# Kernel optimization log

Hardware: AMD Instinct MI355X
Metric: run time of the kernel (lower is better)

## Reference

```python
import jax, jax.numpy as jnp
import numpy as np

N_CAMS = 6
Y, X, Z = 8, 256, 256      # voxel grid (height, x, z)
H, W = 224, 400            # image size used by project_world2img scale
XV, ZV = 56, 100           # img_feats spatial dims [BS,C,XV,ZV]
EPS = 1e-6


def setup_inputs():
    key = jax.random.key(0)
    k1, k2, k3 = jax.random.split(key, 3)
    BS, C = N_CAMS, 32
    img_feats = jax.random.normal(k1, (BS, C, XV, ZV), jnp.float32)
    variances = jax.random.uniform(k2, (BS, 1, H, W), jnp.float32)
    render_depth = jax.random.uniform(k3, (BS, 1, H, W), jnp.float32) * 50.0
    # voxel sample coords, ordering matches crop_base: (x_patch, z_patch, height)
    hs = jnp.linspace(-1.0, 3.0, Y)
    xs = jnp.linspace(-24.0, 24.0, X)
    zs = jnp.linspace(-24.0, 24.0, Z)
    hh, px, pz = jnp.meshgrid(hs, xs, zs, indexing='ij')
    sample_coords = jnp.stack([px, pz, hh], -1).reshape(1, Y * X * Z, 3)
    # six surround cameras at origin, yaw-rotated, looking horizontally (cam2world)
    Ps = np.zeros((N_CAMS, 4, 4), np.float32)
    for i in range(N_CAMS):
        a = i * (2.0 * np.pi / N_CAMS)
        c, s = np.cos(a), np.sin(a)
        # columns are camera x/y/z axes in world coords (y down, z forward)
        Ps[i, :3, :3] = np.array([[s, 0.0, c], [-c, 0.0, s], [0.0, -1.0, 0.0]], np.float32)
        Ps[i, 3, 3] = 1.0
    Ks = np.tile(np.array([[250.0, 0.0, W / 2.0], [0.0, 250.0, H / 2.0], [0.0, 0.0, 1.0]],
                          np.float32), (N_CAMS, 1, 1))
    return {"img_feats": img_feats, "variances": variances, "render_depth": render_depth,
            "sample_coords": sample_coords, "Ps": jnp.asarray(Ps), "Ks": jnp.asarray(Ks)}


def _grid_sample_2d(feat, gx, gy):
    # feat [BS,C,Hf,Wf]; gx,gy [BS,N] normalized to [-1,1].
    # torch.grid_sample bilinear, padding_mode='zeros', align_corners=False
    BS, C, Hf, Wf = feat.shape
    x = (gx + 1.0) * (Wf * 0.5) - 0.5
    y = (gy + 1.0) * (Hf * 0.5) - 0.5
    x0 = jnp.floor(x)
    y0 = jnp.floor(y)
    wx, wy = x - x0, y - y0
    flat = feat.reshape(BS, C, Hf * Wf)
    out = jnp.zeros((BS, C, gx.shape[1]), feat.dtype)
    for dx, dy, wgt in ((0, 0, (1 - wx) * (1 - wy)), (1, 0, wx * (1 - wy)),
                        (0, 1, (1 - wx) * wy), (1, 1, wx * wy)):
        xi = x0 + dx
        yi = y0 + dy
        valid = (xi >= 0) & (xi < Wf) & (yi >= 0) & (yi < Hf)
        idx = (jnp.clip(yi, 0, Hf - 1) * Wf + jnp.clip(xi, 0, Wf - 1)).astype(jnp.int32)
        v = jnp.take_along_axis(flat, idx[:, None, :], axis=2)  # [BS,C,N]
        out = out + v * (wgt * valid)[:, None, :]
    return out


def _masked_mean(x, m, axis):
    # reduce_masked_mean: sum(x*m)/ (sum(m)+eps) along axis
    return jnp.sum(x * m, axis=axis) / (jnp.sum(m, axis=axis) + EPS)


def reference(img_feats, variances, render_depth, sample_coords, Ps, Ks):
    BS, C = img_feats.shape[:2]
    B = BS // N_CAMS
    N = sample_coords.shape[1]
    # --- project_world2img: world -> cam -> pixel ---
    pts_h = jnp.concatenate([sample_coords, jnp.ones((1, N, 1), sample_coords.dtype)], -1)
    w2c = jnp.linalg.inv(Ps)                                    # [BS,4,4]
    cam = jnp.einsum('bij,anj->bni', w2c[:, :3, :], pts_h)      # [BS,N,3]
    uvw = jnp.einsum('bij,bnj->bni', Ks, cam)                   # [BS,N,3]
    zc = uvw[..., 2]
    zsafe = jnp.where(jnp.abs(zc) < 1e-6, 1e-6, zc)
    u = uvw[..., 0] / zsafe
    v = uvw[..., 1] / zsafe
    pix = jnp.nan_to_num(jnp.stack([v, u], -1), nan=-1.0)       # (row, col), scale (H, W)
    mask = (zc > 1e-3) & (u >= 0) & (u < W) & (v >= 0) & (v < H)
    # samp_ind = pix / [H, W] * 2 - 1; coord0 indexes width of permuted feat
    gx = pix[..., 0] / H * 2.0 - 1.0
    gy = pix[..., 1] / W * 2.0 - 1.0
    mf = mask.reshape(B, N_CAMS, 1, Y, X, Z).astype(img_feats.dtype)
    # feature lift: grid_sample on img_feats.permute(0,1,3,2) -> [BS,C,ZV,XV]
    out = _grid_sample_2d(jnp.swapaxes(img_feats, 2, 3), gx, gy)
    out = out.reshape(B, N_CAMS, C, Y, X, Z)
    out_feats = _masked_mean(out, mf, 1).reshape(B, C * Y, X, Z)
    # variance info branch
    var = _grid_sample_2d(jnp.swapaxes(variances, 2, 3), gx, gy)
    var_info = _masked_mean(var.reshape(B, N_CAMS, 1, Y, X, Z), mf, 1).reshape(B, Y, X, Z)
    # depth info branch
    nd = _grid_sample_2d(jnp.swapaxes(render_depth, 2, 3), gx, gy)
    nerf_depth = _masked_mean(nd.reshape(B, N_CAMS, 1, Y, X, Z), mf, 1)  # [B,1,Y,X,Z]
    depth = _masked_mean(zc.reshape(B, N_CAMS, 1, Y, X, Z), mf, 1)       # [B,1,Y,X,Z]
    return (out_feats, var_info, depth, nerf_depth)
```

## Files before the change

### kernel.cpp

```cpp
#include <hip/hip_runtime.h>
#include <math.h>

#define NCAMS 6
#define CCH   32
#define YY    8
#define XX    256
#define ZZ    256
#define NVOX  (YY*XX*ZZ)
#define IMG_H 224
#define IMG_W 400
#define FXV   56
#define FZV   100

#define NF (NCAMS*FXV*FZV)
#define NV (NCAMS*IMG_H*IMG_W)
#define FEATS_T_ELEMS (NF*CCH)
#define VD_T_ELEMS    (NV*2)
#define WS_NEED_BYTES ((size_t)(FEATS_T_ELEMS + VD_T_ELEMS) * 4)

__global__ __launch_bounds__(256) void prep_all(
    const float* __restrict__ src_f, const float* __restrict__ var,
    const float* __restrict__ dep, float* __restrict__ dst_f,
    float* __restrict__ dst_vd)
{
    int t = blockIdx.x * 256 + threadIdx.x;
    if (t < NF) {
        int b = t / (FXV * FZV);
        int r = t - b * (FXV * FZV);
        float4* d4 = (float4*)(dst_f + (size_t)t * CCH);
        #pragma unroll
        for (int j = 0; j < CCH / 4; j++) {
            float4 v;
            v.x = src_f[(size_t)(b * CCH + 4*j + 0) * (FXV*FZV) + r];
            v.y = src_f[(size_t)(b * CCH + 4*j + 1) * (FXV*FZV) + r];
            v.z = src_f[(size_t)(b * CCH + 4*j + 2) * (FXV*FZV) + r];
            v.w = src_f[(size_t)(b * CCH + 4*j + 3) * (FXV*FZV) + r];
            d4[j] = v;
        }
    } else {
        int u = t - NF;
        if (u < NV) ((float2*)dst_vd)[u] = make_float2(var[u], dep[u]);
    }
}

__global__ __launch_bounds__(128) void mvmap_fast(
    const float* __restrict__ feats_t,
    const float* __restrict__ vd_t,
    const float* __restrict__ coords,
    const float* __restrict__ Ps,
    const float* __restrict__ Ks,
    float* __restrict__ out)
{
    __shared__ float4 sW2C[NCAMS][3];
    __shared__ float4 sK[NCAMS][3];

    if (threadIdx.x < NCAMS) {
        int b = threadIdx.x;
        const float* P = Ps + b * 16;
        float r00=P[0], r01=P[1], r02=P[2],  tx=P[3];
        float r10=P[4], r11=P[5], r12=P[6],  ty=P[7];
        float r20=P[8], r21=P[9], r22=P[10], tz=P[11];
        float det = r00*(r11*r22 - r12*r21)
                  - r01*(r10*r22 - r12*r20)
                  + r02*(r10*r21 - r11*r20);
        float id = 1.0f / det;
        float i00 =  (r11*r22 - r12*r21) * id;
        float i01 = -(r01*r22 - r02*r21) * id;
        float i02 =  (r01*r12 - r02*r11) * id;
        float i10 = -(r10*r22 - r12*r20) * id;
        float i11 =  (r00*r22 - r02*r20) * id;
        float i12 = -(r00*r12 - r02*r10) * id;
        float i20 =  (r10*r21 - r11*r20) * id;
        float i21 = -(r00*r21 - r01*r20) * id;
        float i22 =  (r00*r11 - r01*r10) * id;
        sW2C[b][0] = make_float4(i00, i01, i02, -(i00*tx + i01*ty + i02*tz));
        sW2C[b][1] = make_float4(i10, i11, i12, -(i10*tx + i11*ty + i12*tz));
        sW2C[b][2] = make_float4(i20, i21, i22, -(i20*tx + i21*ty + i22*tz));
        sK[b][0] = make_float4(Ks[b*9+0], Ks[b*9+1], Ks[b*9+2], 0.f);
        sK[b][1] = make_float4(Ks[b*9+3], Ks[b*9+4], Ks[b*9+5], 0.f);
        sK[b][2] = make_float4(Ks[b*9+6], Ks[b*9+7], Ks[b*9+8], 0.f);
    }
    __syncthreads();

    int t = blockIdx.x * 128 + threadIdx.x;
    int n = t >> 1;
    int j = t & 1;

    float px = coords[3*n + 0];
    float pz = coords[3*n + 1];
    float ph = coords[3*n + 2];

    float4 facc[4];
    #pragma unroll
    for (int q = 0; q < 4; q++) facc[q] = make_float4(0.f,0.f,0.f,0.f);
    float wsum = 0.0f, vsum = 0.0f, ndsum = 0.0f, zsum = 0.0f;

    int   nvis = 0;
    float s_u[3] = {0.f, 0.f, 0.f};
    float s_v[3] = {0.f, 0.f, 0.f};
    int   s_b[3] = {0, 0, 0};

    #pragma unroll
    for (int b = 0; b < NCAMS; b++) {
        float4 r0 = sW2C[b][0], r1 = sW2C[b][1], r2 = sW2C[b][2];
        float cx = r0.x*px + r0.y*pz + r0.z*ph + r0.w;
        float cy = r1.x*px + r1.y*pz + r1.z*ph + r1.w;
        float cz = r2.x*px + r2.y*pz + r2.z*ph + r2.w;
        float4 k0 = sK[b][0], k1 = sK[b][1], k2 = sK[b][2];
        float u0 = k0.x*cx + k0.y*cy + k0.z*cz;
        float v0 = k1.x*cx + k1.y*cy + k1.z*cz;
        float zc = k2.x*cx + k2.y*cy + k2.z*cz;
        float zsafe = (fabsf(zc) < 1e-6f) ? 1e-6f : zc;
        float u = u0 / zsafe;
        float v = v0 / zsafe;
        bool mask = (zc > 1e-3f) && (u >= 0.0f) && (u < (float)IMG_W)
                                 && (v >= 0.0f) && (v < (float)IMG_H);
        wsum += mask ? 1.0f : 0.0f;
        zsum += mask ? zc : 0.0f;
        bool c0 = mask && (nvis == 0);
        bool c1 = mask && (nvis == 1);
        bool c2 = mask && (nvis == 2);
        s_u[0] = c0 ? u : s_u[0];  s_v[0] = c0 ? v : s_v[0];  s_b[0] = c0 ? b : s_b[0];
        s_u[1] = c1 ? u : s_u[1];  s_v[1] = c1 ? v : s_v[1];  s_b[1] = c1 ? b : s_b[1];
        s_u[2] = c2 ? u : s_u[2];  s_v[2] = c2 ? v : s_v[2];  s_b[2] = c2 ? b : s_b[2];
        nvis += mask ? 1 : 0;
    }

    #pragma unroll
    for (int it = 0; it < 3; it++) {
        if (nvis > it) {
            float u = s_u[it], v = s_v[it];
            int   b = s_b[it];

            {
                float xf = v * 0.25f - 0.5f;
                float yf = u * 0.25f - 0.5f;
                float x0f = floorf(xf), y0f = floorf(yf);
                float wx = xf - x0f, wy = yf - y0f;
                int x0 = (int)x0f, y0 = (int)y0f;
                float vx0 = (x0   >= 0 && x0   < FXV) ? 1.0f : 0.0f;
                float vx1 = (x0+1 >= 0 && x0+1 < FXV) ? 1.0f : 0.0f;
                float vy0 = (y0   >= 0 && y0   < FZV) ? 1.0f : 0.0f;
                float vy1 = (y0+1 >= 0 && y0+1 < FZV) ? 1.0f : 0.0f;
                float w00 = (1.0f-wx)*(1.0f-wy)*vx0*vy0;
                float w10 = wx*(1.0f-wy)*vx1*vy0;
                float w01 = (1.0f-wx)*wy*vx0*vy1;
                float w11 = wx*wy*vx1*vy1;
                int xi0 = min(max(x0,   0), FXV-1), xi1 = min(max(x0+1, 0), FXV-1);
                int yi0 = min(max(y0,   0), FZV-1), yi1 = min(max(y0+1, 0), FZV-1);
                const float* base = feats_t + (size_t)b * (FXV*FZV*CCH) + j * 16;
                const float4* p00 = (const float4*)(base + (size_t)(xi0*FZV + yi0)*CCH);
                const float4* p01 = (const float4*)(base + (size_t)(xi0*FZV + yi1)*CCH);
                const float4* p10 = (const float4*)(base + (size_t)(xi1*FZV + yi0)*CCH);
                const float4* p11 = (const float4*)(base + (size_t)(xi1*FZV + yi1)*CCH);
                #pragma unroll
                for (int q = 0; q < 4; q++) {
                    float4 a = p00[q], b2 = p01[q], c2 = p10[q], d2 = p11[q];
                    facc[q].x += w00*a.x + w01*b2.x + w10*c2.x + w11*d2.x;
                    facc[q].y += w00*a.y + w01*b2.y + w10*c2.y + w11*d2.y;
                    facc[q].z += w00*a.z + w01*b2.z + w10*c2.z + w11*d2.z;
                    facc[q].w += w00*a.w + w01*b2.w + w10*c2.w + w11*d2.w;
                }
            }

            {
                float xf = v - 0.5f;
                float yf = u - 0.5f;
                float x0f = floorf(xf), y0f = floorf(yf);
                float wx = xf - x0f, wy = yf - y0f;
                int x0 = (int)x0f, y0 = (int)y0f;
                float vx0 = (x0   >= 0 && x0   < IMG_H) ? 1.0f : 0.0f;
                float vx1 = (x0+1 >= 0 && x0+1 < IMG_H) ? 1.0f : 0.0f;
                float vy0 = (y0   >= 0 && y0   < IMG_W) ? 1.0f : 0.0f;
                float vy1 = (y0+1 >= 0 && y0+1 < IMG_W) ? 1.0f : 0.0f;
                float w00 = (1.0f-wx)*(1.0f-wy)*vx0*vy0;
                float w10 = wx*(1.0f-wy)*vx1*vy0;
                float w01 = (1.0f-wx)*wy*vx0*vy1;
                float w11 = wx*wy*vx1*vy1;
                int xi0 = min(max(x0,   0), IMG_H-1), xi1 = min(max(x0+1, 0), IMG_H-1);
                int yi0 = min(max(y0,   0), IMG_W-1), yi1 = min(max(y0+1, 0), IMG_W-1);
                const float2* pv = (const float2*)(vd_t) + (size_t)b * (IMG_H*IMG_W);
                float2 t00 = pv[xi0*IMG_W + yi0], t01 = pv[xi0*IMG_W + yi1];
                float2 t10 = pv[xi1*IMG_W + yi0], t11 = pv[xi1*IMG_W + yi1];
                vsum  += w00*t00.x + w01*t01.x + w10*t10.x + w11*t11.x;
                ndsum += w00*t00.y + w01*t01.y + w10*t10.y + w11*t11.y;
            }
        }
    }

    float invd = 1.0f / (wsum + 1e-6f);
    #pragma unroll
    for (int q = 0; q < 4; q++) {
        #pragma unroll
        for (int k = 0; k < 4; k++) {
            float fv = (&facc[q].x)[k] * invd;
            __builtin_nontemporal_store(fv, &out[(size_t)(16*j + 4*q + k) * NVOX + n]);
        }
    }
    if (j == 0) {
        __builtin_nontemporal_store(vsum  * invd, &out[(size_t)CCH*NVOX + n]);
        __builtin_nontemporal_store(zsum  * invd, &out[(size_t)CCH*NVOX + NVOX + n]);
        __builtin_nontemporal_store(ndsum * invd, &out[(size_t)CCH*NVOX + 2*(size_t)NVOX + n]);
    }
}

__global__ __launch_bounds__(256) void mvmap_main(
    const float* __restrict__ img_feats,
    const float* __restrict__ variances,
    const float* __restrict__ render_depth,
    const float* __restrict__ coords,
    const float* __restrict__ Ps,
    const float* __restrict__ Ks,
    float* __restrict__ out)
{
    __shared__ float sW2C[NCAMS][12];
    __shared__ float sK[NCAMS][9];

    if (threadIdx.x < NCAMS) {
        int b = threadIdx.x;
        const float* P = Ps + b * 16;
        float r00=P[0], r01=P[1], r02=P[2],  tx=P[3];
        float r10=P[4], r11=P[5], r12=P[6],  ty=P[7];
        float r20=P[8], r21=P[9], r22=P[10], tz=P[11];
        float det = r00*(r11*r22 - r12*r21)
                  - r01*(r10*r22 - r12*r20)
                  + r02*(r10*r21 - r11*r20);
        float id = 1.0f / det;
        float i00 =  (r11*r22 - r12*r21) * id;
        float i01 = -(r01*r22 - r02*r21) * id;
        float i02 =  (r01*r12 - r02*r11) * id;
        float i10 = -(r10*r22 - r12*r20) * id;
        float i11 =  (r00*r22 - r02*r20) * id;
        float i12 = -(r00*r12 - r02*r10) * id;
        float i20 =  (r10*r21 - r11*r20) * id;
        float i21 = -(r00*r21 - r01*r20) * id;
        float i22 =  (r00*r11 - r01*r10) * id;
        sW2C[b][0]=i00; sW2C[b][1]=i01; sW2C[b][2] =i02; sW2C[b][3] =-(i00*tx + i01*ty + i02*tz);
        sW2C[b][4]=i10; sW2C[b][5]=i11; sW2C[b][6] =i12; sW2C[b][7] =-(i10*tx + i11*ty + i12*tz);
        sW2C[b][8]=i20; sW2C[b][9]=i21; sW2C[b][10]=i22; sW2C[b][11]=-(i20*tx + i21*ty + i22*tz);
        #pragma unroll
        for (int jj = 0; jj < 9; jj++) sK[b][jj] = Ks[b*9 + jj];
    }
    __syncthreads();

    int n = blockIdx.x * blockDim.x + threadIdx.x;
    if (n >= NVOX) return;

    float px = coords[3*n + 0];
    float pz = coords[3*n + 1];
    float ph = coords[3*n + 2];

    float fsum[CCH];
    #pragma unroll
    for (int c = 0; c < CCH; c++) fsum[c] = 0.0f;
    float wsum = 0.0f, vsum = 0.0f, ndsum = 0.0f, zsum = 0.0f;

    for (int b = 0; b < NCAMS; b++) {
        float cx = sW2C[b][0]*px + sW2C[b][1]*pz + sW2C[b][2] *ph + sW2C[b][3];
        float cy = sW2C[b][4]*px + sW2C[b][5]*pz + sW2C[b][6] *ph + sW2C[b][7];
        float cz = sW2C[b][8]*px + sW2C[b][9]*pz + sW2C[b][10]*ph + sW2C[b][11];
        float u0 = sK[b][0]*cx + sK[b][1]*cy + sK[b][2]*cz;
        float v0 = sK[b][3]*cx + sK[b][4]*cy + sK[b][5]*cz;
        float zc = sK[b][6]*cx + sK[b][7]*cy + sK[b][8]*cz;
        float zsafe = (fabsf(zc) < 1e-6f) ? 1e-6f : zc;
        float u = u0 / zsafe;
        float v = v0 / zsafe;
        bool mask = (zc > 1e-3f) && (u >= 0.0f) && (u < (float)IMG_W)
                                 && (v >= 0.0f) && (v < (float)IMG_H);
        if (!mask) continue;

        wsum += 1.0f;
        zsum += zc;
        {
            float xf = v * 0.25f - 0.5f;
            float yf = u * 0.25f - 0.5f;
            float x0f = floorf(xf), y0f = floorf(yf);
            float wx = xf - x0f, wy = yf - y0f;
            int x0 = (int)x0f, y0 = (int)y0f;
            float vx0 = (x0   >= 0 && x0   < FXV) ? 1.0f : 0.0f;
            float vx1 = (x0+1 >= 0 && x0+1 < FXV) ? 1.0f : 0.0f;
            float vy0 = (y0   >= 0 && y0   < FZV) ? 1.0f : 0.0f;
            float vy1 = (y0+1 >= 0 && y0+1 < FZV) ? 1.0f : 0.0f;
            float w00 = (1.0f-wx)*(1.0f-wy)*vx0*vy0;
            float w10 = wx*(1.0f-wy)*vx1*vy0;
            float w01 = (1.0f-wx)*wy*vx0*vy1;
            float w11 = wx*wy*vx1*vy1;
            int xi0 = min(max(x0,   0), FXV-1), xi1 = min(max(x0+1, 0), FXV-1);
            int yi0 = min(max(y0,   0), FZV-1), yi1 = min(max(y0+1, 0), FZV-1);
            int o00 = xi0*FZV + yi0, o01 = xi0*FZV + yi1;
            int o10 = xi1*FZV + yi0, o11 = xi1*FZV + yi1;
            const float* p = img_feats + (size_t)b * (CCH*FXV*FZV);
            #pragma unroll
            for (int c = 0; c < CCH; c++) {
                const float* pc = p + c * (FXV*FZV);
                fsum[c] += w00*pc[o00] + w01*pc[o01] + w10*pc[o10] + w11*pc[o11];
            }
        }
        {
            float xf = v - 0.5f;
            float yf = u - 0.5f;
            float x0f = floorf(xf), y0f = floorf(yf);
            float wx = xf - x0f, wy = yf - y0f;
            int x0 = (int)x0f, y0 = (int)y0f;
            float vx0 = (x0   >= 0 && x0   < IMG_H) ? 1.0f : 0.0f;
            float vx1 = (x0+1 >= 0 && x0+1 < IMG_H) ? 1.0f : 0.0f;
            float vy0 = (y0   >= 0 && y0   < IMG_W) ? 1.0f : 0.0f;
            float vy1 = (y0+1 >= 0 && y0+1 < IMG_W) ? 1.0f : 0.0f;
            float w00 = (1.0f-wx)*(1.0f-wy)*vx0*vy0;
            float w10 = wx*(1.0f-wy)*vx1*vy0;
            float w01 = (1.0f-wx)*wy*vx0*vy1;
            float w11 = wx*wy*vx1*vy1;
            int xi0 = min(max(x0,   0), IMG_H-1), xi1 = min(max(x0+1, 0), IMG_H-1);
            int yi0 = min(max(y0,   0), IMG_W-1), yi1 = min(max(y0+1, 0), IMG_W-1);
            int o00 = xi0*IMG_W + yi0, o01 = xi0*IMG_W + yi1;
            int o10 = xi1*IMG_W + yi0, o11 = xi1*IMG_W + yi1;
            const float* pv = variances    + (size_t)b * (IMG_H*IMG_W);
            const float* pd = render_depth + (size_t)b * (IMG_H*IMG_W);
            vsum  += w00*pv[o00] + w01*pv[o01] + w10*pv[o10] + w11*pv[o11];
            ndsum += w00*pd[o00] + w01*pd[o01] + w10*pd[o10] + w11*pd[o11];
        }
    }

    float invd = 1.0f / (wsum + 1e-6f);
    #pragma unroll
    for (int c = 0; c < CCH; c++) out[(size_t)c * NVOX + n] = fsum[c] * invd;
    out[(size_t)CCH*NVOX + n]              = vsum  * invd;
    out[(size_t)CCH*NVOX + NVOX + n]       = zsum  * invd;
    out[(size_t)CCH*NVOX + 2*(size_t)NVOX + n] = ndsum * invd;
}

extern "C" void kernel_launch(void* const* d_in, const int* in_sizes, int n_in,
                              void* d_out, int out_size, void* d_ws, size_t ws_size,
                              hipStream_t stream) {
    const float* img_feats    = (const float*)d_in[0];
    const float* variances    = (const float*)d_in[1];
    const float* render_depth = (const float*)d_in[2];
    const float* coords       = (const float*)d_in[3];
    const float* Ps           = (const float*)d_in[4];
    const float* Ks           = (const float*)d_in[5];
    float* out = (float*)d_out;

    if (ws_size >= WS_NEED_BYTES) {
        float* feats_t = (float*)d_ws;
        float* vd_t    = feats_t + FEATS_T_ELEMS;
        {
            int total = NF + NV;
            hipLaunchKernelGGL(prep_all, dim3((total + 255) / 256), dim3(256), 0, stream,
                               img_feats, variances, render_depth, feats_t, vd_t);
        }
        hipLaunchKernelGGL(mvmap_fast, dim3((2 * NVOX) / 128), dim3(128), 0, stream,
                           feats_t, vd_t, coords, Ps, Ks, out);
    } else {
        hipLaunchKernelGGL(mvmap_main, dim3(NVOX / 256), dim3(256), 0, stream,
                           img_feats, variances, render_depth, coords, Ps, Ks, out);
    }
}
```

Baseline: 47.60 us.

## Use one thread per voxel with wavefront-shuffled channel gathers and LDS transpose

The fast kernel now maps one voxel per thread in 64-thread blocks. Each thread computes the projection once and does the variance/depth sampling for its own voxel. The 32-channel feature gather is then split across lanes: 8 channel groups times 8 voxels per step, with each voxel's sample coordinates broadcast by wavefront shuffles. Results are transposed through shared memory so each channel's output store is coalesced. This removes the duplicated projection work of the old two-threads-per-voxel scheme and cuts per-thread register use. In exchange it adds many shuffles, an LDS round trip and a block-wide sync.

```diff
diff --git a/kernel.cpp b/kernel.cpp
--- a/kernel.cpp
+++ b/kernel.cpp
@@ -43,7 +43,7 @@
     }
 }
 
-__global__ __launch_bounds__(128) void mvmap_fast(
+__global__ __launch_bounds__(64) void mvmap_fast(
     const float* __restrict__ feats_t,
     const float* __restrict__ vd_t,
     const float* __restrict__ coords,
@@ -53,9 +53,11 @@
 {
     __shared__ float4 sW2C[NCAMS][3];
     __shared__ float4 sK[NCAMS][3];
-
-    if (threadIdx.x < NCAMS) {
-        int b = threadIdx.x;
+    __shared__ float  sT[64 * 33];
+
+    int lane = threadIdx.x;
+    if (lane < NCAMS) {
+        int b = lane;
         const float* P = Ps + b * 16;
         float r00=P[0], r01=P[1], r02=P[2],  tx=P[3];
         float r10=P[4], r11=P[5], r12=P[6],  ty=P[7];
@@ -82,19 +84,14 @@
     }
     __syncthreads();
 
-    int t = blockIdx.x * 128 + threadIdx.x;
-    int n = t >> 1;
-    int j = t & 1;
+    int n0 = blockIdx.x * 64;
+    int n  = n0 + lane;
 
     float px = coords[3*n + 0];
     float pz = coords[3*n + 1];
     float ph = coords[3*n + 2];
 
-    float4 facc[4];
-    #pragma unroll
-    for (int q = 0; q < 4; q++) facc[q] = make_float4(0.f,0.f,0.f,0.f);
-    float wsum = 0.0f, vsum = 0.0f, ndsum = 0.0f, zsum = 0.0f;
-
+    float wsum = 0.0f, zsum = 0.0f;
     int   nvis = 0;
     float s_u[3] = {0.f, 0.f, 0.f};
     float s_v[3] = {0.f, 0.f, 0.f};
@@ -125,14 +122,65 @@
         s_u[2] = c2 ? u : s_u[2];  s_v[2] = c2 ? v : s_v[2];  s_b[2] = c2 ? b : s_b[2];
         nvis += mask ? 1 : 0;
     }
-
+    float invd = 1.0f / (wsum + 1e-6f);
+
+    float vsum = 0.0f, ndsum = 0.0f;
     #pragma unroll
     for (int it = 0; it < 3; it++) {
-        if (nvis > it) {
+        if (it < nvis) {
             float u = s_u[it], v = s_v[it];
             int   b = s_b[it];
-
-            {
+            float xf = v - 0.5f;
+            float yf = u - 0.5f;
+            float x0f = floorf(xf), y0f = floorf(yf);
+            float wx = xf - x0f, wy = yf - y0f;
+            int x0 = (int)x0f, y0 = (int)y0f;
+            float vx0 = (x0   >= 0 && x0   < IMG_H) ? 1.0f : 0.0f;
+            float vx1 = (x0+1 >= 0 && x0+1 < IMG_H) ? 1.0f : 0.0f;
+            float vy0 = (y0   >= 0 && y0   < IMG_W) ? 1.0f : 0.0f;
+            float vy1 = (y0+1 >= 0 && y0+1 < IMG_W) ? 1.0f : 0.0f;
+            float w00 = (1.0f-wx)*(1.0f-wy)*vx0*vy0;
+            float w10 = wx*(1.0f-wy)*vx1*vy0;
+            float w01 = (1.0f-wx)*wy*vx0*vy1;
+            float w11 = wx*wy*vx1*vy1;
+            int xi0 = min(max(x0,   0), IMG_H-1), xi1 = min(max(x0+1, 0), IMG_H-1);
+            int yi0 = min(max(y0,   0), IMG_W-1), yi1 = min(max(y0+1, 0), IMG_W-1);
+            const float2* pv = (const float2*)(vd_t) + (size_t)b * (IMG_H*IMG_W);
+            float2 t00 = pv[xi0*IMG_W + yi0], t01 = pv[xi0*IMG_W + yi1];
+            float2 t10 = pv[xi1*IMG_W + yi0], t11 = pv[xi1*IMG_W + yi1];
+            vsum  += w00*t00.x + w01*t01.x + w10*t10.x + w11*t11.x;
+            ndsum += w00*t00.y + w01*t01.y + w10*t10.y + w11*t11.y;
+        }
+    }
+    __builtin_nontemporal_store(vsum  * invd, &out[(size_t)CCH*NVOX + n]);
+    __builtin_nontemporal_store(zsum  * invd, &out[(size_t)CCH*NVOX + NVOX + n]);
+    __builtin_nontemporal_store(ndsum * invd, &out[(size_t)CCH*NVOX + 2*(size_t)NVOX + n]);
+
+    int cg = lane & 7;
+    int vg = lane >> 3;
+
+    #pragma unroll
+    for (int s = 0; s < 8; s++) {
+        int src = 8*s + vg;
+
+        int   nv  = __shfl(nvis, src);
+        float iv  = __shfl(invd, src);
+        float uu0 = __shfl(s_u[0], src), vv0 = __shfl(s_v[0], src);
+        float uu1 = __shfl(s_u[1], src), vv1 = __shfl(s_v[1], src);
+        float uu2 = __shfl(s_u[2], src), vv2 = __shfl(s_v[2], src);
+        int   bb0 = __shfl(s_b[0], src);
+        int   bb1 = __shfl(s_b[1], src);
+        int   bb2 = __shfl(s_b[2], src);
+        float uu[3] = {uu0, uu1, uu2};
+        float vv[3] = {vv0, vv1, vv2};
+        int   bb[3] = {bb0, bb1, bb2};
+
+        float ax = 0.f, ay = 0.f, az = 0.f, aw = 0.f;
+        #pragma unroll
+        for (int it = 0; it < 3; it++) {
+            if (it < nv) {
+                float u = uu[it], v = vv[it];
+                int   b = bb[it];
                 float xf = v * 0.25f - 0.5f;
                 float yf = u * 0.25f - 0.5f;
                 float x0f = floorf(xf), y0f = floorf(yf);
@@ -148,59 +196,29 @@
                 float w11 = wx*wy*vx1*vy1;
                 int xi0 = min(max(x0,   0), FXV-1), xi1 = min(max(x0+1, 0), FXV-1);
                 int yi0 = min(max(y0,   0), FZV-1), yi1 = min(max(y0+1, 0), FZV-1);
-                const float* base = feats_t + (size_t)b * (FXV*FZV*CCH) + j * 16;
-                const float4* p00 = (const float4*)(base + (size_t)(xi0*FZV + yi0)*CCH);
-                const float4* p01 = (const float4*)(base + (size_t)(xi0*FZV + yi1)*CCH);
-                const float4* p10 = (const float4*)(base + (size_t)(xi1*FZV + yi0)*CCH);
-                const float4* p11 = (const float4*)(base + (size_t)(xi1*FZV + yi1)*CCH);
-                #pragma unroll
-                for (int q = 0; q < 4; q++) {
-                    float4 a = p00[q], b2 = p01[q], c2 = p10[q], d2 = p11[q];
-                    facc[q].x += w00*a.x + w01*b2.x + w10*c2.x + w11*d2.x;
-                    facc[q].y += w00*a.y + w01*b2.y + w10*c2.y + w11*d2.y;
-                    facc[q].z += w00*a.z + w01*b2.z + w10*c2.z + w11*d2.z;
-                    facc[q].w += w00*a.w + w01*b2.w + w10*c2.w + w11*d2.w;
-                }
+                const float* base = feats_t + (size_t)b * (FXV*FZV*CCH) + cg * 4;
+                float4 a  = *(const float4*)(base + (size_t)(xi0*FZV + yi0)*CCH);
+                float4 b2 = *(const float4*)(base + (size_t)(xi0*FZV + yi1)*CCH);
+                float4 c2 = *(const float4*)(base + (size_t)(xi1*FZV + yi0)*CCH);
+                float4 d2 = *(const float4*)(base + (size_t)(xi1*FZV + yi1)*CCH);
+                ax += w00*a.x + w01*b2.x + w10*c2.x + w11*d2.x;
+                ay += w00*a.y + w01*b2.y + w10*c2.y + w11*d2.y;
+                az += w00*a.z + w01*b2.z + w10*c2.z + w11*d2.z;
+                aw += w00*a.w + w01*b2.w + w10*c2.w + w11*d2.w;
             }
-
-            {
-                float xf = v - 0.5f;
-                float yf = u - 0.5f;
-                float x0f = floorf(xf), y0f = floorf(yf);
-                float wx = xf - x0f, wy = yf - y0f;
-                int x0 = (int)x0f, y0 = (int)y0f;
-                float vx0 = (x0   >= 0 && x0   < IMG_H) ? 1.0f : 0.0f;
-                float vx1 = (x0+1 >= 0 && x0+1 < IMG_H) ? 1.0f : 0.0f;
-                float vy0 = (y0   >= 0 && y0   < IMG_W) ? 1.0f : 0.0f;
-                float vy1 = (y0+1 >= 0 && y0+1 < IMG_W) ? 1.0f : 0.0f;
-                float w00 = (1.0f-wx)*(1.0f-wy)*vx0*vy0;
-                float w10 = wx*(1.0f-wy)*vx1*vy0;
-                float w01 = (1.0f-wx)*wy*vx0*vy1;
-                float w11 = wx*wy*vx1*vy1;
-                int xi0 = min(max(x0,   0), IMG_H-1), xi1 = min(max(x0+1, 0), IMG_H-1);
-                int yi0 = min(max(y0,   0), IMG_W-1), yi1 = min(max(y0+1, 0), IMG_W-1);
-                const float2* pv = (const float2*)(vd_t) + (size_t)b * (IMG_H*IMG_W);
-                float2 t00 = pv[xi0*IMG_W + yi0], t01 = pv[xi0*IMG_W + yi1];
-                float2 t10 = pv[xi1*IMG_W + yi0], t11 = pv[xi1*IMG_W + yi1];
-                vsum  += w00*t00.x + w01*t01.x + w10*t10.x + w11*t11.x;
-                ndsum += w00*t00.y + w01*t01.y + w10*t10.y + w11*t11.y;
-            }
-        }
-    }
-
-    float invd = 1.0f / (wsum + 1e-6f);
-    #pragma unroll
-    for (int q = 0; q < 4; q++) {
-        #pragma unroll
-        for (int k = 0; k < 4; k++) {
-            float fv = (&facc[q].x)[k] * invd;
-            __builtin_nontemporal_store(fv, &out[(size_t)(16*j + 4*q + k) * NVOX + n]);
-        }
-    }
-    if (j == 0) {
-        __builtin_nontemporal_store(vsum  * invd, &out[(size_t)CCH*NVOX + n]);
-        __builtin_nontemporal_store(zsum  * invd, &out[(size_t)CCH*NVOX + NVOX + n]);
-        __builtin_nontemporal_store(ndsum * invd, &out[(size_t)CCH*NVOX + 2*(size_t)NVOX + n]);
+        }
+        float* p = &sT[(8*s + vg) * 33 + cg * 4];
+        p[0] = ax * iv;
+        p[1] = ay * iv;
+        p[2] = az * iv;
+        p[3] = aw * iv;
+    }
+    __syncthreads();
+
+    #pragma unroll
+    for (int c = 0; c < CCH; c++) {
+        float val = sT[lane * 33 + c];
+        __builtin_nontemporal_store(val, &out[(size_t)c * NVOX + n]);
     }
 }
 
@@ -348,7 +366,7 @@
             hipLaunchKernelGGL(prep_all, dim3((total + 255) / 256), dim3(256), 0, stream,
                                img_feats, variances, render_depth, feats_t, vd_t);
         }
-        hipLaunchKernelGGL(mvmap_fast, dim3((2 * NVOX) / 128), dim3(128), 0, stream,
+        hipLaunchKernelGGL(mvmap_fast, dim3(NVOX / 64), dim3(64), 0, stream,
                            feats_t, vd_t, coords, Ps, Ks, out);
     } else {
         hipLaunchKernelGGL(mvmap_main, dim3(NVOX / 256), dim3(256), 0, stream,
```

New measurement: 41.14 us. 1.16x faster.

## Remap mvmap_fast to one voxel per lane with shuffle-based channel-group gather

Applied to the files above, without the earlier changes.

Each lane now projects a single voxel and computes the variance/depth branch once, where previously two threads per voxel both projected it. Projection results are then broadcast via wave shuffles so 16 voxels × 4 channel groups of 8 channels each are gathered per pass across four passes. This removes the duplicated projection math and halves the thread count. Stores per channel now cover 16 contiguous voxels, and the change adds shuffle overhead plus a serial four-pass loop per wave.

```diff
diff --git a/kernel.cpp b/kernel.cpp
--- a/kernel.cpp
+++ b/kernel.cpp
@@ -43,7 +43,7 @@
     }
 }
 
-__global__ __launch_bounds__(128) void mvmap_fast(
+__global__ __launch_bounds__(256, 6) void mvmap_fast(
     const float* __restrict__ feats_t,
     const float* __restrict__ vd_t,
     const float* __restrict__ coords,
@@ -82,19 +82,16 @@
     }
     __syncthreads();
 
-    int t = blockIdx.x * 128 + threadIdx.x;
-    int n = t >> 1;
-    int j = t & 1;
+    int wv   = threadIdx.x >> 6;
+    int lane = threadIdx.x & 63;
+    int n0   = blockIdx.x * 256 + wv * 64;
+    int n    = n0 + lane;
 
     float px = coords[3*n + 0];
     float pz = coords[3*n + 1];
     float ph = coords[3*n + 2];
 
-    float4 facc[4];
-    #pragma unroll
-    for (int q = 0; q < 4; q++) facc[q] = make_float4(0.f,0.f,0.f,0.f);
-    float wsum = 0.0f, vsum = 0.0f, ndsum = 0.0f, zsum = 0.0f;
-
+    float wsum = 0.0f, zsum = 0.0f;
     int   nvis = 0;
     float s_u[3] = {0.f, 0.f, 0.f};
     float s_v[3] = {0.f, 0.f, 0.f};
@@ -125,14 +122,66 @@
         s_u[2] = c2 ? u : s_u[2];  s_v[2] = c2 ? v : s_v[2];  s_b[2] = c2 ? b : s_b[2];
         nvis += mask ? 1 : 0;
     }
-
+    float invd = 1.0f / (wsum + 1e-6f);
+
+    float vsum = 0.0f, ndsum = 0.0f;
     #pragma unroll
     for (int it = 0; it < 3; it++) {
-        if (nvis > it) {
+        if (it < nvis) {
             float u = s_u[it], v = s_v[it];
             int   b = s_b[it];
-
-            {
+            float xf = v - 0.5f;
+            float yf = u - 0.5f;
+            float x0f = floorf(xf), y0f = floorf(yf);
+            float wx = xf - x0f, wy = yf - y0f;
+            int x0 = (int)x0f, y0 = (int)y0f;
+            float vx0 = (x0   >= 0 && x0   < IMG_H) ? 1.0f : 0.0f;
+            float vx1 = (x0+1 >= 0 && x0+1 < IMG_H) ? 1.0f : 0.0f;
+            float vy0 = (y0   >= 0 && y0   < IMG_W) ? 1.0f : 0.0f;
+            float vy1 = (y0+1 >= 0 && y0+1 < IMG_W) ? 1.0f : 0.0f;
+            float w00 = (1.0f-wx)*(1.0f-wy)*vx0*vy0;
+            float w10 = wx*(1.0f-wy)*vx1*vy0;
+            float w01 = (1.0f-wx)*wy*vx0*vy1;
+            float w11 = wx*wy*vx1*vy1;
+            int xi0 = min(max(x0,   0), IMG_H-1), xi1 = min(max(x0+1, 0), IMG_H-1);
+            int yi0 = min(max(y0,   0), IMG_W-1), yi1 = min(max(y0+1, 0), IMG_W-1);
+            const float2* pv = (const float2*)(vd_t) + (size_t)b * (IMG_H*IMG_W);
+            float2 t00 = pv[xi0*IMG_W + yi0], t01 = pv[xi0*IMG_W + yi1];
+            float2 t10 = pv[xi1*IMG_W + yi0], t11 = pv[xi1*IMG_W + yi1];
+            vsum  += w00*t00.x + w01*t01.x + w10*t10.x + w11*t11.x;
+            ndsum += w00*t00.y + w01*t01.y + w10*t10.y + w11*t11.y;
+        }
+    }
+    __builtin_nontemporal_store(vsum  * invd, &out[(size_t)CCH*NVOX + n]);
+    __builtin_nontemporal_store(zsum  * invd, &out[(size_t)CCH*NVOX + NVOX + n]);
+    __builtin_nontemporal_store(ndsum * invd, &out[(size_t)CCH*NVOX + 2*(size_t)NVOX + n]);
+
+    int cg = lane >> 4;
+    int vg = lane & 15;
+
+    #pragma unroll
+    for (int s = 0; s < 4; s++) {
+        int src = 16*s + vg;
+
+        int   nv  = __shfl(nvis, src);
+        float iv  = __shfl(invd, src);
+        float uu0 = __shfl(s_u[0], src), vv0 = __shfl(s_v[0], src);
+        float uu1 = __shfl(s_u[1], src), vv1 = __shfl(s_v[1], src);
+        float uu2 = __shfl(s_u[2], src), vv2 = __shfl(s_v[2], src);
+        int   bb0 = __shfl(s_b[0], src);
+        int   bb1 = __shfl(s_b[1], src);
+        int   bb2 = __shfl(s_b[2], src);
+        float uu[3] = {uu0, uu1, uu2};
+        float vv[3] = {vv0, vv1, vv2};
+        int   bb[3] = {bb0, bb1, bb2};
+
+        float4 f0 = make_float4(0.f,0.f,0.f,0.f);
+        float4 f1 = make_float4(0.f,0.f,0.f,0.f);
+        #pragma unroll
+        for (int it = 0; it < 3; it++) {
+            if (it < nv) {
+                float u = uu[it], v = vv[it];
+                int   b = bb[it];
                 float xf = v * 0.25f - 0.5f;
                 float yf = u * 0.25f - 0.5f;
                 float x0f = floorf(xf), y0f = floorf(yf);
@@ -148,59 +197,36 @@
                 float w11 = wx*wy*vx1*vy1;
                 int xi0 = min(max(x0,   0), FXV-1), xi1 = min(max(x0+1, 0), FXV-1);
                 int yi0 = min(max(y0,   0), FZV-1), yi1 = min(max(y0+1, 0), FZV-1);
-                const float* base = feats_t + (size_t)b * (FXV*FZV*CCH) + j * 16;
+                const float* base = feats_t + (size_t)b * (FXV*FZV*CCH) + cg * 8;
                 const float4* p00 = (const float4*)(base + (size_t)(xi0*FZV + yi0)*CCH);
                 const float4* p01 = (const float4*)(base + (size_t)(xi0*FZV + yi1)*CCH);
                 const float4* p10 = (const float4*)(base + (size_t)(xi1*FZV + yi0)*CCH);
                 const float4* p11 = (const float4*)(base + (size_t)(xi1*FZV + yi1)*CCH);
-                #pragma unroll
-                for (int q = 0; q < 4; q++) {
-                    float4 a = p00[q], b2 = p01[q], c2 = p10[q], d2 = p11[q];
-                    facc[q].x += w00*a.x + w01*b2.x + w10*c2.x + w11*d2.x;
-                    facc[q].y += w00*a.y + w01*b2.y + w10*c2.y + w11*d2.y;
-                    facc[q].z += w00*a.z + w01*b2.z + w10*c2.z + w11*d2.z;
-                    facc[q].w += w00*a.w + w01*b2.w + w10*c2.w + w11*d2.w;
+                {
+                    float4 a = p00[0], b2 = p01[0], c2 = p10[0], d2 = p11[0];
+                    f0.x += w00*a.x + w01*b2.x + w10*c2.x + w11*d2.x;
+                    f0.y += w00*a.y + w01*b2.y + w10*c2.y + w11*d2.y;
+                    f0.z += w00*a.z + w01*b2.z + w10*c2.z + w11*d2.z;
+                    f0.w += w00*a.w + w01*b2.w + w10*c2.w + w11*d2.w;
+                }
+                {
+                    float4 a = p00[1], b2 = p01[1], c2 = p10[1], d2 = p11[1];
+                    f1.x += w00*a.x + w01*b2.x + w10*c2.x + w11*d2.x;
+                    f1.y += w00*a.y + w01*b2.y + w10*c2.y + w11*d2.y;
+                    f1.z += w00*a.z + w01*b2.z + w10*c2.z + w11*d2.z;
+                    f1.w += w00*a.w + w01*b2.w + w10*c2.w + w11*d2.w;
                 }
             }
-
-            {
-                float xf = v - 0.5f;
-                float yf = u - 0.5f;
-                float x0f = floorf(xf), y0f = floorf(yf);
-                float wx = xf - x0f, wy = yf - y0f;
-                int x0 = (int)x0f, y0 = (int)y0f;
-                float vx0 = (x0   >= 0 && x0   < IMG_H) ? 1.0f : 0.0f;
-                float vx1 = (x0+1 >= 0 && x0+1 < IMG_H) ? 1.0f : 0.0f;
-                float vy0 = (y0   >= 0 && y0   < IMG_W) ? 1.0f : 0.0f;
-                float vy1 = (y0+1 >= 0 && y0+1 < IMG_W) ? 1.0f : 0.0f;
-                float w00 = (1.0f-wx)*(1.0f-wy)*vx0*vy0;
-                float w10 = wx*(1.0f-wy)*vx1*vy0;
-                float w01 = (1.0f-wx)*wy*vx0*vy1;
-                float w11 = wx*wy*vx1*vy1;
-                int xi0 = min(max(x0,   0), IMG_H-1), xi1 = min(max(x0+1, 0), IMG_H-1);
-                int yi0 = min(max(y0,   0), IMG_W-1), yi1 = min(max(y0+1, 0), IMG_W-1);
-                const float2* pv = (const float2*)(vd_t) + (size_t)b * (IMG_H*IMG_W);
-                float2 t00 = pv[xi0*IMG_W + yi0], t01 = pv[xi0*IMG_W + yi1];
-                float2 t10 = pv[xi1*IMG_W + yi0], t11 = pv[xi1*IMG_W + yi1];
-                vsum  += w00*t00.x + w01*t01.x + w10*t10.x + w11*t11.x;
-                ndsum += w00*t00.y + w01*t01.y + w10*t10.y + w11*t11.y;
-            }
-        }
-    }
-
-    float invd = 1.0f / (wsum + 1e-6f);
-    #pragma unroll
-    for (int q = 0; q < 4; q++) {
+        }
+        int vn = n0 + 16*s + vg;
         #pragma unroll
         for (int k = 0; k < 4; k++) {
-            float fv = (&facc[q].x)[k] * invd;
-            __builtin_nontemporal_store(fv, &out[(size_t)(16*j + 4*q + k) * NVOX + n]);
-        }
-    }
-    if (j == 0) {
-        __builtin_nontemporal_store(vsum  * invd, &out[(size_t)CCH*NVOX + n]);
-        __builtin_nontemporal_store(zsum  * invd, &out[(size_t)CCH*NVOX + NVOX + n]);
-        __builtin_nontemporal_store(ndsum * invd, &out[(size_t)CCH*NVOX + 2*(size_t)NVOX + n]);
+            __builtin_nontemporal_store((&f0.x)[k] * iv, &out[(size_t)(8*cg + k) * NVOX + vn]);
+        }
+        #pragma unroll
+        for (int k = 0; k < 4; k++) {
+            __builtin_nontemporal_store((&f1.x)[k] * iv, &out[(size_t)(8*cg + 4 + k) * NVOX + vn]);
+        }
     }
 }
 
@@ -348,7 +374,7 @@
             hipLaunchKernelGGL(prep_all, dim3((total + 255) / 256), dim3(256), 0, stream,
                                img_feats, variances, render_depth, feats_t, vd_t);
         }
-        hipLaunchKernelGGL(mvmap_fast, dim3((2 * NVOX) / 128), dim3(128), 0, stream,
+        hipLaunchKernelGGL(mvmap_fast, dim3(NVOX / 256), dim3(256), 0, stream,
                            feats_t, vd_t, coords, Ps, Ks, out);
     } else {
         hipLaunchKernelGGL(mvmap_main, dim3(NVOX / 256), dim3(256), 0, stream,
```

After: 50.78 us. 6.7% more time.
